# Kernel tuning notes

Measured on AMD Instinct MI355X. Metric: run time of the kernel, lower is better.

## Reference

```python
import jax, jax.numpy as jnp
import numpy as np
import math

C = 1024
CH = C // 2


def setup_inputs() -> dict:
    key = jax.random.key(0)
    ks = jax.random.split(key, 8)
    B, Nq, Nk = 8, 2048, 2048
    y = jax.random.normal(ks[0], (B, Nq, C), dtype=jnp.float32)
    x = jax.random.normal(ks[1], (B, Nk, C), dtype=jnp.float32)
    # torch nn.Linear weights are [out, in]; custom normal init per module
    Wq = jax.random.normal(ks[2], (CH, C), dtype=jnp.float32) * math.sqrt(2.0 / CH)
    Wk = jax.random.normal(ks[3], (CH, C), dtype=jnp.float32) * math.sqrt(2.0 / CH)
    Wv = jax.random.normal(ks[4], (C, C), dtype=jnp.float32) * math.sqrt(2.0 / C)
    # biases keep default torch Linear init: U(-1/sqrt(in), 1/sqrt(in))
    b = 1.0 / math.sqrt(C)
    bq = jax.random.uniform(ks[5], (CH,), minval=-b, maxval=b, dtype=jnp.float32)
    bk = jax.random.uniform(ks[6], (CH,), minval=-b, maxval=b, dtype=jnp.float32)
    bv = jax.random.uniform(ks[7], (C,), minval=-b, maxval=b, dtype=jnp.float32)
    return {"y": y, "x": x, "Wq": Wq, "bq": bq, "Wk": Wk, "bk": bk, "Wv": Wv, "bv": bv}


def reference(y, x, Wq, bq, Wk, bk, Wv, bv):
    scale = (C // 2) ** (-0.5)
    q = jnp.einsum('bnc,hc->bnh', y, Wq) + bq          # [B, Nq, C/2]
    k = jnp.einsum('bmc,hc->bmh', x, Wk) + bk          # [B, Nk, C/2]
    v = jnp.einsum('bmc,dc->bmd', x, Wv) + bv          # [B, Nk, C]
    dots = jnp.einsum('bnh,bmh->bnm', q, k) * scale    # [B, Nq, Nk]
    attn = jax.nn.softmax(dots, axis=-2)               # softmax over QUERY dim
    out = jnp.einsum('bnm,bmd->bnd', attn, v)          # [B, Nq, C]
    return out
```

## Files before the change

kernel.cpp:

```cpp
#include <hip/hip_runtime.h>
#include <hip/hip_bf16.h>


using bf16 = __bf16;
typedef __attribute__((ext_vector_type(8))) __bf16 bf16x8;
typedef __attribute__((ext_vector_type(4))) float f32x4;

#define GLB_AS __attribute__((address_space(1)))
#define LDS_AS __attribute__((address_space(3)))

__device__ __forceinline__ void gload_lds16(const void* g, void* l) {
  __builtin_amdgcn_global_load_lds((const GLB_AS uint32_t*)g,
                                   (LDS_AS uint32_t*)l, 16, 0, 0);
}

#define BAR() __builtin_amdgcn_s_barrier()
#define LGK0() asm volatile("s_waitcnt lgkmcnt(0)" ::: "memory")
#define VM8() asm volatile("s_waitcnt vmcnt(8)" ::: "memory")

enum { EPI_BIAS = 0, EPI_EXP = 1, EPI_OUT = 2 };

template <int EPI>
__global__ __launch_bounds__(512, 2) void gemm256(
    const bf16* __restrict__ A, const bf16* __restrict__ Bt,
    void* __restrict__ Cv, const float* __restrict__ bias,
    float* __restrict__ Z, int M, int N, int K, int ldA, int ldB, int ldC,
    long sA, long sB, long sC, float scale) {
  __shared__ __align__(16) bf16 As[4 * 8192];
  __shared__ __align__(16) bf16 Bs[4 * 8192];

  const int bz = blockIdx.z;
  const bf16* Ab = A + (long)bz * sA;
  const bf16* Bb = Bt + (long)bz * sB;

  const int tid = threadIdx.x;
  const int lane = tid & 63;
  const int wave = tid >> 6;
  const int wr = wave >> 2;
  const int wc = wave & 3;
  const int fl = lane & 15;
  const int kg = lane >> 4;
  const long m0 = (long)blockIdx.x * 256;
  const long n0 = (long)blockIdx.y * 256;

  f32x4 acc[8][4] = {};

  const int srow = tid >> 2;
  const int scol = (tid & 3) * 8;
  const bf16* gA0 = Ab + (m0 + srow) * (long)ldA + scol;
  const bf16* gA1 = Ab + (m0 + 128 + srow) * (long)ldA + scol;
  const bf16* gB0 = Bb + (n0 + srow) * (long)ldB + scol;
  const bf16* gB1 = Bb + (n0 + 128 + srow) * (long)ldB + scol;
  const int l0 = tid * 8, l1 = 4096 + tid * 8;

  const int nt = K >> 5;

#define STAGE_A(tt)                                    \
  {                                                    \
    const int _b = ((tt) & 3) * 8192;                  \
    const long _k = (long)(tt) * 32;                   \
    gload_lds16(gA0 + _k, &As[_b + l0]);               \
    gload_lds16(gA1 + _k, &As[_b + l1]);               \
  }
#define STAGE_B(tt)                                    \
  {                                                    \
    const int _b = ((tt) & 3) * 8192;                  \
    const long _k = (long)(tt) * 32;                   \
    gload_lds16(gB0 + _k, &Bs[_b + l0]);               \
    gload_lds16(gB1 + _k, &Bs[_b + l1]);               \
  }
#define RD_A(bo, i, mh) \
  (*(const bf16x8*)&As[(bo) + (wr * 128 + (mh)*64 + (i)*16 + fl) * 32 + kg * 8])
#define RD_B(bo, j) \
  (*(const bf16x8*)&Bs[(bo) + (wc * 64 + (j)*16 + fl) * 32 + kg * 8])

  STAGE_A(0) STAGE_B(0) STAGE_A(1) STAGE_B(1) STAGE_A(2) STAGE_B(2)
  VM8();
  BAR();

  for (int t = 0; t < nt; ++t) {
    const int bo = (t & 3) * 8192;
    const int tt = t + 3;
    bf16x8 a0, a1, a2, a3, b0, b1, b2, b3;
    a0 = RD_A(bo, 0, 0); a1 = RD_A(bo, 1, 0);
    a2 = RD_A(bo, 2, 0); a3 = RD_A(bo, 3, 0);
    b0 = RD_B(bo, 0); b1 = RD_B(bo, 1); b2 = RD_B(bo, 2); b3 = RD_B(bo, 3);
    if (tt < nt) STAGE_A(tt);
    BAR();
    LGK0();
    __builtin_amdgcn_s_setprio(1);
#pragma unroll
    for (int j = 0; j < 4; j++) {
      acc[0][j] = __builtin_amdgcn_mfma_f32_16x16x32_bf16(a0, j == 0 ? b0 : j == 1 ? b1 : j == 2 ? b2 : b3, acc[0][j], 0, 0, 0);
      acc[1][j] = __builtin_amdgcn_mfma_f32_16x16x32_bf16(a1, j == 0 ? b0 : j == 1 ? b1 : j == 2 ? b2 : b3, acc[1][j], 0, 0, 0);
      acc[2][j] = __builtin_amdgcn_mfma_f32_16x16x32_bf16(a2, j == 0 ? b0 : j == 1 ? b1 : j == 2 ? b2 : b3, acc[2][j], 0, 0, 0);
      acc[3][j] = __builtin_amdgcn_mfma_f32_16x16x32_bf16(a3, j == 0 ? b0 : j == 1 ? b1 : j == 2 ? b2 : b3, acc[3][j], 0, 0, 0);
    }
    __builtin_amdgcn_s_setprio(0);
    BAR();
    a0 = RD_A(bo, 0, 1); a1 = RD_A(bo, 1, 1);
    a2 = RD_A(bo, 2, 1); a3 = RD_A(bo, 3, 1);
    if (tt < nt) STAGE_B(tt);
    BAR();
    LGK0();
    __builtin_amdgcn_s_setprio(1);
#pragma unroll
    for (int j = 0; j < 4; j++) {
      acc[4][j] = __builtin_amdgcn_mfma_f32_16x16x32_bf16(a0, j == 0 ? b0 : j == 1 ? b1 : j == 2 ? b2 : b3, acc[4][j], 0, 0, 0);
      acc[5][j] = __builtin_amdgcn_mfma_f32_16x16x32_bf16(a1, j == 0 ? b0 : j == 1 ? b1 : j == 2 ? b2 : b3, acc[5][j], 0, 0, 0);
      acc[6][j] = __builtin_amdgcn_mfma_f32_16x16x32_bf16(a2, j == 0 ? b0 : j == 1 ? b1 : j == 2 ? b2 : b3, acc[6][j], 0, 0, 0);
      acc[7][j] = __builtin_amdgcn_mfma_f32_16x16x32_bf16(a3, j == 0 ? b0 : j == 1 ? b1 : j == 2 ? b2 : b3, acc[7][j], 0, 0, 0);
    }
    __builtin_amdgcn_s_setprio(0);
    VM8();
    BAR();
  }
#undef STAGE_A
#undef STAGE_B
#undef RD_A
#undef RD_B

  if constexpr (EPI == EPI_BIAS) {
    bf16* Cb = (bf16*)Cv + (long)bz * sC;
#pragma unroll
    for (int j = 0; j < 4; j++) {
      const long cc = n0 + wc * 64 + j * 16 + fl;
      const float bc = bias[cc];
#pragma unroll
      for (int mi = 0; mi < 8; mi++)
#pragma unroll
        for (int e = 0; e < 4; e++) {
          const long rr = m0 + wr * 128 + mi * 16 + kg * 4 + e;
          Cb[rr * ldC + cc] = (bf16)(acc[mi][j][e] + bc);
        }
    }
  } else if constexpr (EPI == EPI_EXP) {
    bf16* Cb = (bf16*)Cv + (long)bz * sC;
    float* Zb = Z + (long)bz * N;
#pragma unroll
    for (int j = 0; j < 4; j++) {
      const long cc = n0 + wc * 64 + j * 16 + fl;
      float zp = 0.f;
#pragma unroll
      for (int mi = 0; mi < 8; mi++)
#pragma unroll
        for (int e = 0; e < 4; e++) {
          const long rr = m0 + wr * 128 + mi * 16 + kg * 4 + e;
          const float ex = __expf(acc[mi][j][e] * scale);
          zp += ex;
          Cb[rr * ldC + cc] = (bf16)ex;
        }
      atomicAdd(&Zb[cc], zp);
    }
  } else {
    float* Cb = (float*)Cv + (long)bz * sC;
#pragma unroll
    for (int j = 0; j < 4; j++) {
      const long cc = n0 + wc * 64 + j * 16 + fl;
#pragma unroll
      for (int mi = 0; mi < 8; mi++)
#pragma unroll
        for (int e = 0; e < 4; e++) {
          const long rr = m0 + wr * 128 + mi * 16 + kg * 4 + e;
          Cb[rr * ldC + cc] = acc[mi][j][e];
        }
    }
  }
}

__global__ void cvt_f32_bf16(const float* __restrict__ in,
                             bf16* __restrict__ out, long n4) {
  long i = blockIdx.x * (long)blockDim.x + threadIdx.x;
  const long stride = (long)gridDim.x * blockDim.x;
  for (; i < n4; i += stride) {
    const float4 f = ((const float4*)in)[i];
    union { ushort4 u; bf16 h[4]; } p;
    p.h[0] = (bf16)f.x;
    p.h[1] = (bf16)f.y;
    p.h[2] = (bf16)f.z;
    p.h[3] = (bf16)f.w;
    ((ushort4*)out)[i] = p.u;
  }
}

__global__ __launch_bounds__(256) void transpose_scale(
    const bf16* __restrict__ kv, const float* __restrict__ Z,
    bf16* __restrict__ vt) {
  __shared__ bf16 tile[32][33];
  const int b = blockIdx.z;
  const bf16* vb = kv + (long)b * 2048 * 1536 + 512;
  bf16* vtb = vt + (long)b * 1024 * 2048;
  const float* Zb = Z + b * 2048;
  const int m0 = blockIdx.x * 32, d0 = blockIdx.y * 32;
  const int t = threadIdx.x;
  const int r = t >> 3, c4 = (t & 7) * 4;

  union { ushort4 u; bf16 h[4]; } in;
  in.u = *(const ushort4*)&vb[(long)(m0 + r) * 1536 + d0 + c4];
  tile[r][c4 + 0] = in.h[0];
  tile[r][c4 + 1] = in.h[1];
  tile[r][c4 + 2] = in.h[2];
  tile[r][c4 + 3] = in.h[3];
  __syncthreads();

  union { ushort4 u; bf16 h[4]; } o;
#pragma unroll
  for (int j = 0; j < 4; j++)
    o.h[j] = (bf16)((float)tile[c4 + j][r] / Zb[m0 + c4 + j]);
  *(ushort4*)&vtb[(long)(d0 + r) * 2048 + m0 + c4] = o.u;
}

extern "C" void kernel_launch(void* const* d_in, const int* in_sizes, int n_in,
                              void* d_out, int out_size, void* d_ws,
                              size_t ws_size, hipStream_t stream) {
  const float* y = (const float*)d_in[0];
  const float* x = (const float*)d_in[1];
  const float* Wq = (const float*)d_in[2];
  const float* bq = (const float*)d_in[3];
  const float* Wk = (const float*)d_in[4];
  const float* bk = (const float*)d_in[5];
  const float* Wv = (const float*)d_in[6];
  const float* bv = (const float*)d_in[7];
  float* out = (float*)d_out;

  constexpr long B = 8, Nq = 2048, Nk = 2048, Cd = 1024, CH = 512;
  constexpr long BN = B * Nq;
  const float scale = 0.04419417382415922f;

  char* w = (char*)d_ws;
  auto alloc = [&](size_t bytes) {
    char* p = w;
    w += (bytes + 255) & ~(size_t)255;
    return p;
  };
  bf16* y_bf = (bf16*)alloc(BN * Cd * 2);
  bf16* x_bf = (bf16*)alloc(BN * Cd * 2);
  bf16* Wq_bf = (bf16*)alloc(CH * Cd * 2);
  bf16* Wkv_bf = (bf16*)alloc((CH + Cd) * Cd * 2);
  float* bkv = (float*)alloc((CH + Cd) * 4);
  bf16* q_bf = (bf16*)alloc(BN * CH * 2);
  bf16* kv_bf = (bf16*)alloc(BN * (CH + Cd) * 2);
  bf16* vt_bf = (bf16*)alloc(BN * Cd * 2);
  bf16* P_bf = (bf16*)alloc(B * Nq * Nk * 2);
  float* Zsum = (float*)alloc(B * Nk * 4);
  if ((size_t)(w - (char*)d_ws) > ws_size) return;

  cvt_f32_bf16<<<2048, 256, 0, stream>>>(y, y_bf, BN * Cd / 4);
  cvt_f32_bf16<<<2048, 256, 0, stream>>>(x, x_bf, BN * Cd / 4);
  cvt_f32_bf16<<<512, 256, 0, stream>>>(Wq, Wq_bf, CH * Cd / 4);
  cvt_f32_bf16<<<512, 256, 0, stream>>>(Wk, Wkv_bf, CH * Cd / 4);
  cvt_f32_bf16<<<1024, 256, 0, stream>>>(Wv, Wkv_bf + CH * Cd, Cd * Cd / 4);
  hipMemcpyAsync(bkv, bk, CH * 4, hipMemcpyDeviceToDevice, stream);
  hipMemcpyAsync(bkv + CH, bv, Cd * 4, hipMemcpyDeviceToDevice, stream);

  gemm256<EPI_BIAS><<<dim3(64, 2, 1), 512, 0, stream>>>(
      y_bf, Wq_bf, q_bf, bq, nullptr, BN, CH, Cd, Cd, Cd, CH, 0, 0, 0, 0.f);
  gemm256<EPI_BIAS><<<dim3(64, 6, 1), 512, 0, stream>>>(
      x_bf, Wkv_bf, kv_bf, bkv, nullptr, BN, CH + Cd, Cd, Cd, Cd, CH + Cd,
      0, 0, 0, 0.f);

  hipMemsetAsync(Zsum, 0, B * Nk * 4, stream);
  gemm256<EPI_EXP><<<dim3(8, 8, 8), 512, 0, stream>>>(
      q_bf, kv_bf, P_bf, nullptr, Zsum, Nq, Nk, CH, CH, CH + Cd, Nk,
      Nq * CH, Nk * (CH + Cd), Nq * Nk, scale);

  transpose_scale<<<dim3(64, 32, 8), 256, 0, stream>>>(kv_bf, Zsum, vt_bf);

  gemm256<EPI_OUT><<<dim3(8, 4, 8), 512, 0, stream>>>(
      P_bf, vt_bf, out, nullptr, nullptr, Nq, Cd, Nk, Nk, Nk, Cd,
      Nq * Nk, Cd * Nk, Nq * Cd, 0.f);
}
```

Measured before the change: 479.0 us.

## Swizzle LDS tiles, cut pipeline to three stages, split MFMA phases by B columns

Adds an XOR swizzle to the global-to-LDS staging and the LDS read addresses so that fragment reads avoid bank conflicts. The ring buffer shrinks from four stages to three (prefetch distance two), which lowers LDS use per block. The inner loop now loads all eight A fragments once and splits the two MFMA phases by B column pairs instead of A row halves. This keeps more A registers live and shortens the prefetch lead, so latency hiding may suffer.

```diff
diff --git a/kernel.cpp b/kernel.cpp
--- a/kernel.cpp
+++ b/kernel.cpp
@@ -16,7 +16,8 @@
 
 #define BAR() __builtin_amdgcn_s_barrier()
 #define LGK0() asm volatile("s_waitcnt lgkmcnt(0)" ::: "memory")
-#define VM8() asm volatile("s_waitcnt vmcnt(8)" ::: "memory")
+#define VM4() asm volatile("s_waitcnt vmcnt(4)" ::: "memory")
+#define VM0() asm volatile("s_waitcnt vmcnt(0)" ::: "memory")
 
 enum { EPI_BIAS = 0, EPI_EXP = 1, EPI_OUT = 2 };
 
@@ -26,8 +27,8 @@
     void* __restrict__ Cv, const float* __restrict__ bias,
     float* __restrict__ Z, int M, int N, int K, int ldA, int ldB, int ldC,
     long sA, long sB, long sC, float scale) {
-  __shared__ __align__(16) bf16 As[4 * 8192];
-  __shared__ __align__(16) bf16 Bs[4 * 8192];
+  __shared__ __align__(16) bf16 As[3 * 8192];
+  __shared__ __align__(16) bf16 Bs[3 * 8192];
 
   const int bz = blockIdx.z;
   const bf16* Ab = A + (long)bz * sA;
@@ -45,80 +46,76 @@
 
   f32x4 acc[8][4] = {};
 
-  const int srow = tid >> 2;
-  const int scol = (tid & 3) * 8;
-  const bf16* gA0 = Ab + (m0 + srow) * (long)ldA + scol;
-  const bf16* gA1 = Ab + (m0 + 128 + srow) * (long)ldA + scol;
-  const bf16* gB0 = Bb + (n0 + srow) * (long)ldB + scol;
-  const bf16* gB1 = Bb + (n0 + 128 + srow) * (long)ldB + scol;
-  const int l0 = tid * 8, l1 = 4096 + tid * 8;
+  const int js = tid ^ ((tid >> 3) & 7);
+  const int srow = js >> 2;
+  const int scol = (js & 3) * 8;
+  const bf16* gAc = Ab + (m0 + srow) * (long)ldA + scol;
+  const bf16* gBc = Bb + (n0 + srow) * (long)ldB + scol;
+  char* Abase = (char*)As;
+  char* Bbase = (char*)Bs;
+
+#define STAGE_A(tt)                                         \
+  {                                                         \
+    char* _d = Abase + ((tt) % 3) * 16384 + tid * 16;       \
+    const bf16* _g = gAc + (long)(tt) * 32;                 \
+    gload_lds16(_g, _d);                                    \
+    gload_lds16(_g + 128 * (long)ldA, _d + 8192);           \
+  }
+#define STAGE_B(tt)                                         \
+  {                                                         \
+    char* _d = Bbase + ((tt) % 3) * 16384 + tid * 16;       \
+    const bf16* _g = gBc + (long)(tt) * 32;                 \
+    gload_lds16(_g, _d);                                    \
+    gload_lds16(_g + 128 * (long)ldB, _d + 8192);           \
+  }
+
+  const int swz = (fl >> 1) << 4;
+  const int abase = ((wr * 128 + fl) * 64 + kg * 16) ^ swz;
+  const int bbase = ((wc * 64 + fl) * 64 + kg * 16) ^ swz;
 
   const int nt = K >> 5;
 
-#define STAGE_A(tt)                                    \
-  {                                                    \
-    const int _b = ((tt) & 3) * 8192;                  \
-    const long _k = (long)(tt) * 32;                   \
-    gload_lds16(gA0 + _k, &As[_b + l0]);               \
-    gload_lds16(gA1 + _k, &As[_b + l1]);               \
-  }
-#define STAGE_B(tt)                                    \
-  {                                                    \
-    const int _b = ((tt) & 3) * 8192;                  \
-    const long _k = (long)(tt) * 32;                   \
-    gload_lds16(gB0 + _k, &Bs[_b + l0]);               \
-    gload_lds16(gB1 + _k, &Bs[_b + l1]);               \
-  }
-#define RD_A(bo, i, mh) \
-  (*(const bf16x8*)&As[(bo) + (wr * 128 + (mh)*64 + (i)*16 + fl) * 32 + kg * 8])
-#define RD_B(bo, j) \
-  (*(const bf16x8*)&Bs[(bo) + (wc * 64 + (j)*16 + fl) * 32 + kg * 8])
-
-  STAGE_A(0) STAGE_B(0) STAGE_A(1) STAGE_B(1) STAGE_A(2) STAGE_B(2)
-  VM8();
+  STAGE_A(0) STAGE_B(0) STAGE_A(1) STAGE_B(1)
+  VM4();
   BAR();
 
   for (int t = 0; t < nt; ++t) {
-    const int bo = (t & 3) * 8192;
-    const int tt = t + 3;
-    bf16x8 a0, a1, a2, a3, b0, b1, b2, b3;
-    a0 = RD_A(bo, 0, 0); a1 = RD_A(bo, 1, 0);
-    a2 = RD_A(bo, 2, 0); a3 = RD_A(bo, 3, 0);
-    b0 = RD_B(bo, 0); b1 = RD_B(bo, 1); b2 = RD_B(bo, 2); b3 = RD_B(bo, 3);
-    if (tt < nt) STAGE_A(tt);
+    const char* Asl = Abase + (t % 3) * 16384;
+    const char* Bsl = Bbase + (t % 3) * 16384;
+    bf16x8 a[8], b0, b1;
+#pragma unroll
+    for (int mi = 0; mi < 8; mi++)
+      a[mi] = *(const bf16x8*)(Asl + abase + mi * 1024);
+    b0 = *(const bf16x8*)(Bsl + bbase);
+    b1 = *(const bf16x8*)(Bsl + bbase + 1024);
+    if (t + 2 < nt) STAGE_A(t + 2);
     BAR();
     LGK0();
     __builtin_amdgcn_s_setprio(1);
 #pragma unroll
-    for (int j = 0; j < 4; j++) {
-      acc[0][j] = __builtin_amdgcn_mfma_f32_16x16x32_bf16(a0, j == 0 ? b0 : j == 1 ? b1 : j == 2 ? b2 : b3, acc[0][j], 0, 0, 0);
-      acc[1][j] = __builtin_amdgcn_mfma_f32_16x16x32_bf16(a1, j == 0 ? b0 : j == 1 ? b1 : j == 2 ? b2 : b3, acc[1][j], 0, 0, 0);
-      acc[2][j] = __builtin_amdgcn_mfma_f32_16x16x32_bf16(a2, j == 0 ? b0 : j == 1 ? b1 : j == 2 ? b2 : b3, acc[2][j], 0, 0, 0);
-      acc[3][j] = __builtin_amdgcn_mfma_f32_16x16x32_bf16(a3, j == 0 ? b0 : j == 1 ? b1 : j == 2 ? b2 : b3, acc[3][j], 0, 0, 0);
+    for (int mi = 0; mi < 8; mi++) {
+      acc[mi][0] = __builtin_amdgcn_mfma_f32_16x16x32_bf16(a[mi], b0, acc[mi][0], 0, 0, 0);
+      acc[mi][1] = __builtin_amdgcn_mfma_f32_16x16x32_bf16(a[mi], b1, acc[mi][1], 0, 0, 0);
     }
     __builtin_amdgcn_s_setprio(0);
     BAR();
-    a0 = RD_A(bo, 0, 1); a1 = RD_A(bo, 1, 1);
-    a2 = RD_A(bo, 2, 1); a3 = RD_A(bo, 3, 1);
-    if (tt < nt) STAGE_B(tt);
+    b0 = *(const bf16x8*)(Bsl + bbase + 2 * 1024);
+    b1 = *(const bf16x8*)(Bsl + bbase + 3 * 1024);
+    if (t + 2 < nt) STAGE_B(t + 2);
     BAR();
     LGK0();
     __builtin_amdgcn_s_setprio(1);
 #pragma unroll
-    for (int j = 0; j < 4; j++) {
-      acc[4][j] = __builtin_amdgcn_mfma_f32_16x16x32_bf16(a0, j == 0 ? b0 : j == 1 ? b1 : j == 2 ? b2 : b3, acc[4][j], 0, 0, 0);
-      acc[5][j] = __builtin_amdgcn_mfma_f32_16x16x32_bf16(a1, j == 0 ? b0 : j == 1 ? b1 : j == 2 ? b2 : b3, acc[5][j], 0, 0, 0);
-      acc[6][j] = __builtin_amdgcn_mfma_f32_16x16x32_bf16(a2, j == 0 ? b0 : j == 1 ? b1 : j == 2 ? b2 : b3, acc[6][j], 0, 0, 0);
-      acc[7][j] = __builtin_amdgcn_mfma_f32_16x16x32_bf16(a3, j == 0 ? b0 : j == 1 ? b1 : j == 2 ? b2 : b3, acc[7][j], 0, 0, 0);
+    for (int mi = 0; mi < 8; mi++) {
+      acc[mi][2] = __builtin_amdgcn_mfma_f32_16x16x32_bf16(a[mi], b0, acc[mi][2], 0, 0, 0);
+      acc[mi][3] = __builtin_amdgcn_mfma_f32_16x16x32_bf16(a[mi], b1, acc[mi][3], 0, 0, 0);
     }
     __builtin_amdgcn_s_setprio(0);
-    VM8();
+    if (t + 2 < nt) { VM4(); } else { VM0(); }
     BAR();
   }
 #undef STAGE_A
 #undef STAGE_B
-#undef RD_A
-#undef RD_B
 
   if constexpr (EPI == EPI_BIAS) {
     bf16* Cb = (bf16*)Cv + (long)bz * sC;
```

New measurement: 472.0 us. Within noise of the previous version (-1.5%).
